# Performance work log

Measured on AMD Instinct MI355X. Metric: run time of the kernel, lower is better.

## Reference

```python
import jax, jax.numpy as jnp
import numpy as np

H, W = 512, 512
NUM_CLASSES = 21
THETA_ALPHA, THETA_BETA, THETA_GAMMA = 80.0, 13.0, 3.0
BILATERAL_COMPAT, SPATIAL_COMPAT = 10.0, 3.0
COMPATIBILITY = -1.0
NUM_ITERATIONS = 5


def _find_rows(rows, queries):
    """Index of each query row in `rows` (lexicographically sorted unique), -1 if absent."""
    M = rows.shape[0]
    u, inv = np.unique(np.concatenate([rows, queries], axis=0), axis=0, return_inverse=True)
    table = np.full(u.shape[0], -1, np.int64)
    table[inv[:M]] = np.arange(M)
    return table[inv[M:]].astype(np.int32)


def _perm_init(feats):
    """Permutohedral lattice init (Adams et al.).
    Returns os [N,d+1] (1-based lattice indices, 0 = pad row), ws [N,d+1] barycentric
    weights, nbrs [d+1,M,2] blur neighbor indices (1-based, 0 = missing)."""
    N, d = feats.shape
    inv_std = np.sqrt(2.0 / 3.0) * (d + 1)
    scale = inv_std / np.sqrt((np.arange(1, d + 1) * np.arange(2, d + 2)).astype(np.float64))
    cf = feats.astype(np.float64) * scale[None]
    # Elevate onto the hyperplane sum(x)=0 in d+1 dims
    E = np.zeros((N, d + 1), np.float64)
    sm = np.zeros(N, np.float64)
    for i in range(d, 0, -1):
        E[:, i] = sm - i * cf[:, i - 1]
        sm = sm + cf[:, i - 1]
    E[:, 0] = sm
    down = 1.0 / (d + 1)
    v = E * down
    up_p = np.ceil(v) * (d + 1)
    dn_p = np.floor(v) * (d + 1)
    rem0 = np.where(up_p - E < E - dn_p, up_p, dn_p)  # nearest remainder-0 point
    sum_ = np.round(rem0.sum(1) * down).astype(np.int64)
    diff = E - rem0
    order = np.argsort(-diff, axis=1, kind='stable')
    rank = np.empty((N, d + 1), np.int64)
    np.put_along_axis(rank, order, np.broadcast_to(np.arange(d + 1, dtype=np.int64), (N, d + 1)).copy(), axis=1)
    rank = rank + sum_[:, None]
    ls = rank < 0
    rank = rank + ls * (d + 1); rem0 = rem0 + ls * (d + 1)
    gt = rank > d
    rank = rank - gt * (d + 1); rem0 = rem0 - gt * (d + 1)
    # Barycentric weights
    bary = np.zeros((N, d + 2), np.float64)
    vv = (E - rem0) * down
    rows_idx = np.arange(N)[:, None]
    np.add.at(bary, (rows_idx, d - rank), vv)
    np.add.at(bary, (rows_idx, d + 1 - rank), -vv)
    bary[:, 0] += 1.0 + bary[:, d + 1]
    ws = bary[:, :d + 1].astype(np.float32)
    # Keys of the d+1 enclosing simplex vertices (first d coords only)
    rem0i = np.round(rem0[:, :d]).astype(np.int32)
    ranks = rank[:, :d]
    keys = np.empty((N, d + 1, d), np.int32)
    for k in range(d + 1):
        keys[:, k, :] = rem0i + np.where(ranks < d + 1 - k, k, k - (d + 1)).astype(np.int32)
    uniq, inv = np.unique(keys.reshape(-1, d), axis=0, return_inverse=True)
    M = uniq.shape[0]
    os_ = (inv.reshape(N, d + 1) + 1).astype(np.int32)
    # Blur neighbors along each lattice direction j
    nbrs = np.zeros((d + 1, M, 2), np.int32)
    for j in range(d + 1):
        n1 = uniq - 1; n2 = uniq + 1
        if j < d:
            n1 = n1.copy(); n2 = n2.copy()
            n1[:, j] += d + 1; n2[:, j] -= d + 1
        nbrs[j, :, 0] = _find_rows(uniq, n1) + 1
        nbrs[j, :, 1] = _find_rows(uniq, n2) + 1
    return os_, ws, nbrs


def setup_inputs() -> dict:
    key = jax.random.key(0)
    k1, k2 = jax.random.split(key)
    unary = jax.random.normal(k1, (H, W, NUM_CLASSES), jnp.float32)
    image = jax.random.uniform(k2, (H, W, 3), jnp.float32) * 255.0  # 0..255 like RGB
    ys, xs = np.meshgrid(np.arange(H, dtype=np.float32), np.arange(W, dtype=np.float32), indexing='ij')
    img = np.asarray(image)
    bifeats = np.concatenate([(xs / THETA_ALPHA)[..., None], (ys / THETA_ALPHA)[..., None], img / THETA_BETA], axis=-1).reshape(-1, 5).astype(np.float32)
    spfeats = np.concatenate([(xs / THETA_GAMMA)[..., None], (ys / THETA_GAMMA)[..., None]], axis=-1).reshape(-1, 2).astype(np.float32)
    os_bi, ws_bi, nbr_bi = _perm_init(bifeats)
    os_sp, ws_sp, nbr_sp = _perm_init(spfeats)
    return {
        'unary': unary,
        'ws_bi': jnp.asarray(ws_bi), 'ws_sp': jnp.asarray(ws_sp),
        'os_bi': jnp.asarray(os_bi), 'os_sp': jnp.asarray(os_sp),
        'nbr_bi': jnp.asarray(nbr_bi), 'nbr_sp': jnp.asarray(nbr_sp),
    }


def lattice_compute(inp, os_, ws, nbrs):
    """Permutohedral splat -> blur -> slice. inp [N,C]; os_ [N,d+1] 1-based;
    ws [N,d+1]; nbrs [d+1,M,2] 1-based with 0 = missing (maps to zero pad row)."""
    N, C = inp.shape
    d = os_.shape[1] - 1
    M = nbrs.shape[1]
    splat = (ws[..., None] * inp[:, None, :]).reshape(-1, C)  # [N*(d+1), C]
    val = jnp.zeros((M + 1, C), inp.dtype).at[os_.reshape(-1)].add(splat)

    def blur(val, nbr_j):
        mixed = val[1:] + 0.5 * (val[nbr_j[:, 0]] + val[nbr_j[:, 1]])
        return val.at[1:].set(mixed), None

    val, _ = jax.lax.scan(blur, val, nbrs)
    alpha = 1.0 / (1.0 + 2.0 ** (-d))
    return alpha * jnp.einsum('nj,njc->nc', ws, val[os_])


def reference(unary, ws_bi, ws_sp, os_bi, os_sp, nbr_bi, nbr_sp):
    N = H * W
    u = unary.reshape(N, NUM_CLASSES)
    ones = jnp.ones((N, 1), jnp.float32)
    bi_norm = 1.0 / (lattice_compute(ones, os_bi, ws_bi, nbr_bi) ** 0.5 + 1e-20)
    sp_norm = 1.0 / (lattice_compute(ones, os_sp, ws_sp, nbr_sp) ** 0.5 + 1e-20)
    Q = jax.nn.softmax(-u, axis=-1)
    for _ in range(NUM_ITERATIONS):
        bi = lattice_compute(Q * bi_norm, os_bi, ws_bi, nbr_bi) * bi_norm
        sp = lattice_compute(Q * sp_norm, os_sp, ws_sp, nbr_sp) * sp_norm
        pairwise = COMPATIBILITY * (BILATERAL_COMPAT * bi + SPATIAL_COMPAT * sp)
        Q = jax.nn.softmax(-u - pairwise, axis=-1)
    return Q.reshape(H, W, NUM_CLASSES)
```

## Files before the change

kernel.cpp:

```cpp
#include <hip/hip_runtime.h>
#include <hip/hip_fp16.h>

#define NPIX (512 * 512)
#define LOG2N 18
#define NC 21
#define CP 11
#define SCAN_CHUNK 2048
#define SCAN_T 256

static inline int cdiv_l(long a, int b) { return (int)((a + b - 1) / b); }

__global__ void hist2_k(const int* __restrict__ osA, int* __restrict__ cntA, int NA, int KA,
                        const int* __restrict__ osB, int* __restrict__ cntB, int NB, int KB) {
    int t = blockIdx.x * blockDim.x + threadIdx.x;
    if (t < NA) {
        int j = t >> LOG2N, n = t & (NPIX - 1);
        atomicAdd(&cntA[osA[(size_t)n * KA + j]], 1);
    } else {
        t -= NA;
        if (t < NB) {
            int j = t >> LOG2N, n = t & (NPIX - 1);
            atomicAdd(&cntB[osB[(size_t)n * KB + j]], 1);
        }
    }
}

__global__ void scan1_k(const int* __restrict__ count, int* __restrict__ bsum, int L) {
    __shared__ int s[SCAN_T];
    int base = blockIdx.x * SCAN_CHUNK;
    int tsum = 0;
    for (int j = threadIdx.x; j < SCAN_CHUNK; j += SCAN_T) {
        int i = base + j;
        tsum += (i < L) ? count[i] : 0;
    }
    s[threadIdx.x] = tsum; __syncthreads();
    for (int o = SCAN_T / 2; o > 0; o >>= 1) {
        if (threadIdx.x < o) s[threadIdx.x] += s[threadIdx.x + o];
        __syncthreads();
    }
    if (threadIdx.x == 0) bsum[blockIdx.x] = s[0];
}

__global__ void scan2_k(int* __restrict__ bsum, int nb, int* __restrict__ off, int L) {
    __shared__ int s[SCAN_T];
    int tid = threadIdx.x;
    int per = (nb + SCAN_T - 1) / SCAN_T;
    int tsum = 0;
    for (int j = 0; j < per; j++) { int i = tid * per + j; if (i < nb) tsum += bsum[i]; }
    s[tid] = tsum; __syncthreads();
    for (int o = 1; o < SCAN_T; o <<= 1) {
        int v = (tid >= o) ? s[tid - o] : 0;
        __syncthreads();
        s[tid] += v;
        __syncthreads();
    }
    int excl = s[tid] - tsum;
    int total = s[SCAN_T - 1];
    int run = excl;
    for (int j = 0; j < per; j++) {
        int i = tid * per + j;
        if (i < nb) { int v = bsum[i]; bsum[i] = run; run += v; }
    }
    if (tid == 0) off[L] = total;
}

__global__ void scan3_k(int* __restrict__ count, const int* __restrict__ bsum,
                        int* __restrict__ off, int L) {
    __shared__ int s[SCAN_T];
    const int PER = SCAN_CHUNK / SCAN_T;
    int tid = threadIdx.x;
    int base = blockIdx.x * SCAN_CHUNK + tid * PER;
    int c[PER];
    int tsum = 0;
#pragma unroll
    for (int j = 0; j < PER; j++) { int i = base + j; c[j] = (i < L) ? count[i] : 0; tsum += c[j]; }
    s[tid] = tsum; __syncthreads();
    for (int o = 1; o < SCAN_T; o <<= 1) {
        int v = (tid >= o) ? s[tid - o] : 0;
        __syncthreads();
        s[tid] += v;
        __syncthreads();
    }
    int run = bsum[blockIdx.x] + s[tid] - tsum;
#pragma unroll
    for (int j = 0; j < PER; j++) {
        int i = base + j;
        if (i < L) { off[i] = run; count[i] = 0; }
        run += c[j];
    }
}

__global__ void scatter2_k(const int* __restrict__ osA, const float* __restrict__ wsA,
                           const int* __restrict__ offA, int* __restrict__ curA,
                           int2* __restrict__ pA, int NA, int KA,
                           const int* __restrict__ osB, const float* __restrict__ wsB,
                           const int* __restrict__ offB, int* __restrict__ curB,
                           int2* __restrict__ pB, int NB, int KB) {
    int t = blockIdx.x * blockDim.x + threadIdx.x;
    if (t < NA) {
        int j = t >> LOG2N, n = t & (NPIX - 1);
        size_t e = (size_t)n * KA + j;
        int m = osA[e];
        int p = offA[m] + atomicAdd(&curA[m], 1);
        pA[p] = make_int2(n, __float_as_int(wsA[e]));
    } else {
        t -= NA;
        if (t < NB) {
            int j = t >> LOG2N, n = t & (NPIX - 1);
            size_t e = (size_t)n * KB + j;
            int m = osB[e];
            int p = offB[m] + atomicAdd(&curB[m], 1);
            pB[p] = make_int2(n, __float_as_int(wsB[e]));
        }
    }
}

__global__ void wn2_k(int2* __restrict__ pA, const float* __restrict__ nrmA, int NA,
                      int2* __restrict__ pB, const float* __restrict__ nrmB, int NB) {
    int t = blockIdx.x * blockDim.x + threadIdx.x;
    if (t < NA) {
        int2 e = pA[t];
        e.y = __float_as_int(__int_as_float(e.y) * nrmA[e.x]);
        pA[t] = e;
    } else {
        t -= NA;
        if (t < NB) {
            int2 e = pB[t];
            e.y = __float_as_int(__int_as_float(e.y) * nrmB[e.x]);
            pB[t] = e;
        }
    }
}

__global__ void splat_gather1_k(const int2* __restrict__ pE, const int* __restrict__ off,
                                float* __restrict__ val, int M) {
    int m = blockIdx.x * blockDim.x + threadIdx.x;
    if (m > M) return;
    float s = 0.f;
    if (m > 0) {
        int e0 = off[m], e1 = off[m + 1];
        for (int e = e0; e < e1; e++) s += __int_as_float(pE[e].y);
    }
    val[m] = s;
}

__global__ void blur1_k(const float* __restrict__ vin, float* __restrict__ vout,
                        const int* __restrict__ nbr, int M) {
    int t = blockIdx.x * blockDim.x + threadIdx.x;
    if (t > M) return;
    if (t == 0) { vout[0] = 0.f; return; }
    int2 nn = ((const int2*)nbr)[t - 1];
    vout[t] = vin[t] + 0.5f * (vin[nn.x] + vin[nn.y]);
}

__global__ void slice_norm_k(const float* __restrict__ ws, const int* __restrict__ os,
                             const float* __restrict__ val, float* __restrict__ nrm,
                             int N, int K, float alpha) {
    int n = blockIdx.x * blockDim.x + threadIdx.x;
    if (n >= N) return;
    float s = 0.f;
    for (int j = 0; j < K; j++) s += ws[(size_t)n * K + j] * val[os[(size_t)n * K + j]];
    nrm[n] = 1.f / (sqrtf(alpha * s) + 1e-20f);
}

__global__ void splatH_k(const __half2* __restrict__ Qh, const int2* __restrict__ pE,
                         const int* __restrict__ off, __half2* __restrict__ val, int M) {
    int m = blockIdx.x * blockDim.x + threadIdx.x;
    if (m > M) return;
    float acc[2 * CP];
#pragma unroll
    for (int i = 0; i < 2 * CP; i++) acc[i] = 0.f;
    if (m > 0) {
        int e0 = off[m], e1 = off[m + 1];
        for (int e = e0; e < e1; e++) {
            int2 ent = pE[e];
            float w = __int_as_float(ent.y);
            const __half2* qp = Qh + (size_t)ent.x * CP;
#pragma unroll
            for (int i = 0; i < CP; i++) {
                float2 q = __half22float2(qp[i]);
                acc[2 * i]     += w * q.x;
                acc[2 * i + 1] += w * q.y;
            }
        }
    }
    __half2* vp = val + (size_t)m * CP;
#pragma unroll
    for (int i = 0; i < CP; i++)
        vp[i] = __floats2half2_rn(acc[2 * i], acc[2 * i + 1]);
}

__global__ void blurH_k(const __half2* __restrict__ vin, __half2* __restrict__ vout,
                        const int* __restrict__ nbr, int M) {
    int t = blockIdx.x * blockDim.x + threadIdx.x;
    int total = (M + 1) * CP;
    if (t >= total) return;
    int m = t / CP;
    int cp = t - m * CP;
    if (m == 0) { vout[t] = __floats2half2_rn(0.f, 0.f); return; }
    int2 nn = ((const int2*)nbr)[m - 1];
    float2 a = __half22float2(vin[t]);
    float2 b = __half22float2(vin[(size_t)nn.x * CP + cp]);
    float2 c = __half22float2(vin[(size_t)nn.y * CP + cp]);
    vout[t] = __floats2half2_rn(a.x + 0.5f * (b.x + c.x), a.y + 0.5f * (b.y + c.y));
}

__global__ void blurH2_k(const __half2* __restrict__ vin, __half2* __restrict__ vout,
                         const int* __restrict__ nbrA, const int* __restrict__ nbrB, int M) {
    int m = blockIdx.x * blockDim.x + threadIdx.x;
    if (m > M) return;
    __half2* op = vout + (size_t)m * CP;
    if (m == 0) {
        __half2 z = __floats2half2_rn(0.f, 0.f);
#pragma unroll
        for (int i = 0; i < CP; i++) op[i] = z;
        return;
    }
    float acc[2 * CP];
#pragma unroll
    for (int i = 0; i < 2 * CP; i++) acc[i] = 0.f;
    int2 nbB = ((const int2*)nbrB)[m - 1];

    {
        int2 na = ((const int2*)nbrA)[m - 1];
        const __half2* p0 = vin + (size_t)m * CP;
        const __half2* p1 = vin + (size_t)na.x * CP;
        const __half2* p2 = vin + (size_t)na.y * CP;
#pragma unroll
        for (int i = 0; i < CP; i++) {
            float2 a = __half22float2(p0[i]);
            float2 b = __half22float2(p1[i]);
            float2 c = __half22float2(p2[i]);
            acc[2 * i]     += a.x + 0.5f * (b.x + c.x);
            acc[2 * i + 1] += a.y + 0.5f * (b.y + c.y);
        }
    }
    if (nbB.x > 0) {
        int2 na = ((const int2*)nbrA)[nbB.x - 1];
        const __half2* p0 = vin + (size_t)nbB.x * CP;
        const __half2* p1 = vin + (size_t)na.x * CP;
        const __half2* p2 = vin + (size_t)na.y * CP;
#pragma unroll
        for (int i = 0; i < CP; i++) {
            float2 a = __half22float2(p0[i]);
            float2 b = __half22float2(p1[i]);
            float2 c = __half22float2(p2[i]);
            acc[2 * i]     += 0.5f * (a.x + 0.5f * (b.x + c.x));
            acc[2 * i + 1] += 0.5f * (a.y + 0.5f * (b.y + c.y));
        }
    }
    if (nbB.y > 0) {
        int2 na = ((const int2*)nbrA)[nbB.y - 1];
        const __half2* p0 = vin + (size_t)nbB.y * CP;
        const __half2* p1 = vin + (size_t)na.x * CP;
        const __half2* p2 = vin + (size_t)na.y * CP;
#pragma unroll
        for (int i = 0; i < CP; i++) {
            float2 a = __half22float2(p0[i]);
            float2 b = __half22float2(p1[i]);
            float2 c = __half22float2(p2[i]);
            acc[2 * i]     += 0.5f * (a.x + 0.5f * (b.x + c.x));
            acc[2 * i + 1] += 0.5f * (a.y + 0.5f * (b.y + c.y));
        }
    }
#pragma unroll
    for (int i = 0; i < CP; i++)
        op[i] = __floats2half2_rn(acc[2 * i], acc[2 * i + 1]);
}

__global__ void softmax_init_k(const float* __restrict__ u, __half2* __restrict__ Qh,
                               __half2* __restrict__ uh, int N) {
    int n = blockIdx.x * blockDim.x + threadIdx.x;
    if (n >= N) return;
    const float* up = u + (size_t)n * NC;
    float uv[2 * CP], v[2 * CP];
    float mx = -1e30f;
#pragma unroll
    for (int c = 0; c < NC; c++) { uv[c] = up[c]; v[c] = -uv[c]; mx = fmaxf(mx, v[c]); }
    float s = 0.f;
#pragma unroll
    for (int c = 0; c < NC; c++) { v[c] = __expf(v[c] - mx); s += v[c]; }
    float inv = 1.f / s;
#pragma unroll
    for (int c = 0; c < NC; c++) v[c] *= inv;
    v[NC] = 0.f; uv[NC] = 0.f;
    __half2* hp = Qh + (size_t)n * CP;
    __half2* uhp = uh + (size_t)n * CP;
#pragma unroll
    for (int i = 0; i < CP; i++) {
        hp[i]  = __floats2half2_rn(v[2 * i], v[2 * i + 1]);
        uhp[i] = __floats2half2_rn(uv[2 * i], uv[2 * i + 1]);
    }
}

__global__ void slice_update_k(const __half2* __restrict__ uh,
                               const int* __restrict__ os_bi, const float* __restrict__ ws_bi,
                               const __half2* __restrict__ vbi, const float* __restrict__ nrm_bi,
                               const int* __restrict__ os_sp, const float* __restrict__ ws_sp,
                               const __half2* __restrict__ vsp, const float* __restrict__ nrm_sp,
                               float* __restrict__ Q, __half2* __restrict__ Qh,
                               int N, float abi, float asp, int final_it) {
    int n = blockIdx.x * blockDim.x + threadIdx.x;
    if (n >= N) return;
    float acc[2 * CP];
#pragma unroll
    for (int i = 0; i < 2 * CP; i++) acc[i] = 0.f;
    for (int j = 0; j < 6; j++) {
        float w = ws_bi[(size_t)n * 6 + j];
        const __half2* vp = vbi + (size_t)os_bi[(size_t)n * 6 + j] * CP;
#pragma unroll
        for (int i = 0; i < CP; i++) {
            float2 f = __half22float2(vp[i]);
            acc[2 * i]     += w * f.x;
            acc[2 * i + 1] += w * f.y;
        }
    }
    float sb = 10.f * abi * nrm_bi[n];
#pragma unroll
    for (int i = 0; i < 2 * CP; i++) acc[i] *= sb;
    float ss = 3.f * asp * nrm_sp[n];
    for (int j = 0; j < 3; j++) {
        float w = ss * ws_sp[(size_t)n * 3 + j];
        const __half2* vp = vsp + (size_t)os_sp[(size_t)n * 3 + j] * CP;
#pragma unroll
        for (int i = 0; i < CP; i++) {
            float2 f = __half22float2(vp[i]);
            acc[2 * i]     += w * f.x;
            acc[2 * i + 1] += w * f.y;
        }
    }
    const __half2* uhp = uh + (size_t)n * CP;
#pragma unroll
    for (int i = 0; i < CP; i++) {
        float2 uu = __half22float2(uhp[i]);
        acc[2 * i]     -= uu.x;
        acc[2 * i + 1] -= uu.y;
    }
    float mx = -1e30f;
#pragma unroll
    for (int c = 0; c < NC; c++) mx = fmaxf(mx, acc[c]);
    float s = 0.f;
#pragma unroll
    for (int c = 0; c < NC; c++) { acc[c] = __expf(acc[c] - mx); s += acc[c]; }
    float inv = 1.f / s;
#pragma unroll
    for (int c = 0; c < NC; c++) acc[c] *= inv;
    acc[NC] = 0.f;
    if (final_it) {
        float* qp = Q + (size_t)n * NC;
#pragma unroll
        for (int c = 0; c < NC; c++) qp[c] = acc[c];
    } else {
        __half2* hp = Qh + (size_t)n * CP;
#pragma unroll
        for (int i = 0; i < CP; i++) hp[i] = __floats2half2_rn(acc[2 * i], acc[2 * i + 1]);
    }
}

extern "C" void kernel_launch(void* const* d_in, const int* in_sizes, int n_in,
                              void* d_out, int out_size, void* d_ws, size_t ws_size,
                              hipStream_t stream) {
    const float* unary  = (const float*)d_in[0];
    const float* ws_bi  = (const float*)d_in[1];
    const float* ws_sp  = (const float*)d_in[2];
    const int*   os_bi  = (const int*)d_in[3];
    const int*   os_sp  = (const int*)d_in[4];
    const int*   nbr_bi = (const int*)d_in[5];
    const int*   nbr_sp = (const int*)d_in[6];
    float* Q = (float*)d_out;

    const int N = NPIX, Kbi = 6, Ksp = 3;
    const int Mbi = in_sizes[5] / (Kbi * 2);
    const int Msp = in_sizes[6] / (Ksp * 2);
    const int NKbi = N * Kbi, NKsp = N * Ksp;
    const float alpha_bi = 32.f / 33.f;
    const float alpha_sp = 0.8f;

    char* basec = (char*)d_ws;
    size_t off4 = 0;
    auto allocf = [&](size_t nf) { float* p = (float*)basec + off4; off4 += (nf + 3) & ~(size_t)3; return p; };
    auto alloci = [&](size_t ni) { int* p = (int*)basec + off4; off4 += (ni + 3) & ~(size_t)3; return p; };
    auto alloch2 = [&](size_t nh2) { __half2* p = (__half2*)((float*)basec + off4); off4 += (nh2 + 3) & ~(size_t)3; return p; };
    auto alloci2 = [&](size_t ni2) { int2* p = (int2*)((float*)basec + off4); off4 += 2 * ni2; return p; };

    float*   nrm_bi = allocf(N);
    float*   nrm_sp = allocf(N);
    __half2* Qh     = alloch2((size_t)N * CP);
    __half2* uh     = alloch2((size_t)N * CP);
    int2*    pE_bi  = alloci2(NKbi);
    int*     off_bi = alloci(Mbi + 2);
    int2*    pE_sp  = alloci2(NKsp);
    int*     off_sp = alloci(Msp + 2);
    int*     cur_bi = alloci((size_t)(Mbi + 1) + (Msp + 1));
    int*     cur_sp = cur_bi + (Mbi + 1);
    int*     bsum   = alloci(4096);
    __half2* vbiA   = alloch2((size_t)(Mbi + 1) * CP);
    __half2* vbiB   = alloch2((size_t)(Mbi + 1) * CP);
    __half2* vspA   = alloch2((size_t)(Msp + 1) * CP);
    __half2* vspB   = alloch2((size_t)(Msp + 1) * CP);
    float* nv_biA = (float*)vbiA;
    float* nv_biB = (float*)vbiB;
    float* nv_spA = (float*)vspA;
    float* nv_spB = (float*)vspB;

    const int B = 256;
    const int nb_bi = cdiv_l(Mbi + 1, SCAN_CHUNK);
    const int nb_sp = cdiv_l(Msp + 1, SCAN_CHUNK);
    const size_t cur_span = ((size_t)(Mbi + 1) + (Msp + 1)) * sizeof(int);

    hipMemsetAsync(cur_bi, 0, cur_span, stream);
    hist2_k<<<cdiv_l((long)NKbi + NKsp, B), B, 0, stream>>>(
        os_bi, cur_bi, NKbi, Kbi, os_sp, cur_sp, NKsp, Ksp);
    scan1_k<<<nb_bi, SCAN_T, 0, stream>>>(cur_bi, bsum, Mbi + 1);
    scan2_k<<<1, SCAN_T, 0, stream>>>(bsum, nb_bi, off_bi, Mbi + 1);
    scan3_k<<<nb_bi, SCAN_T, 0, stream>>>(cur_bi, bsum, off_bi, Mbi + 1);
    scan1_k<<<nb_sp, SCAN_T, 0, stream>>>(cur_sp, bsum, Msp + 1);
    scan2_k<<<1, SCAN_T, 0, stream>>>(bsum, nb_sp, off_sp, Msp + 1);
    scan3_k<<<nb_sp, SCAN_T, 0, stream>>>(cur_sp, bsum, off_sp, Msp + 1);
    scatter2_k<<<cdiv_l((long)NKbi + NKsp, B), B, 0, stream>>>(
        os_bi, ws_bi, off_bi, cur_bi, pE_bi, NKbi, Kbi,
        os_sp, ws_sp, off_sp, cur_sp, pE_sp, NKsp, Ksp);

    splat_gather1_k<<<cdiv_l(Mbi + 1, B), B, 0, stream>>>(pE_bi, off_bi, nv_biA, Mbi);
    {
        float* s = nv_biA; float* d = nv_biB;
        for (int j = 0; j < Kbi; j++) {
            blur1_k<<<cdiv_l(Mbi + 1, B), B, 0, stream>>>(s, d, nbr_bi + (size_t)j * Mbi * 2, Mbi);
            float* t = s; s = d; d = t;
        }
        slice_norm_k<<<cdiv_l(N, B), B, 0, stream>>>(ws_bi, os_bi, s, nrm_bi, N, Kbi, alpha_bi);
    }

    splat_gather1_k<<<cdiv_l(Msp + 1, B), B, 0, stream>>>(pE_sp, off_sp, nv_spA, Msp);
    {
        float* s = nv_spA; float* d = nv_spB;
        for (int j = 0; j < Ksp; j++) {
            blur1_k<<<cdiv_l(Msp + 1, B), B, 0, stream>>>(s, d, nbr_sp + (size_t)j * Msp * 2, Msp);
            float* t = s; s = d; d = t;
        }
        slice_norm_k<<<cdiv_l(N, B), B, 0, stream>>>(ws_sp, os_sp, s, nrm_sp, N, Ksp, alpha_sp);
    }

    wn2_k<<<cdiv_l((long)NKbi + NKsp, B), B, 0, stream>>>(pE_bi, nrm_bi, NKbi, pE_sp, nrm_sp, NKsp);

    softmax_init_k<<<cdiv_l(N, B), B, 0, stream>>>(unary, Qh, uh, N);

    for (int it = 0; it < 5; it++) {
        splatH_k<<<cdiv_l(Mbi + 1, B), B, 0, stream>>>(Qh, pE_bi, off_bi, vbiA, Mbi);
        blurH2_k<<<cdiv_l(Mbi + 1, B), B, 0, stream>>>(
            vbiA, vbiB, nbr_bi + (size_t)0 * Mbi * 2, nbr_bi + (size_t)1 * Mbi * 2, Mbi);
        blurH2_k<<<cdiv_l(Mbi + 1, B), B, 0, stream>>>(
            vbiB, vbiA, nbr_bi + (size_t)2 * Mbi * 2, nbr_bi + (size_t)3 * Mbi * 2, Mbi);
        blurH2_k<<<cdiv_l(Mbi + 1, B), B, 0, stream>>>(
            vbiA, vbiB, nbr_bi + (size_t)4 * Mbi * 2, nbr_bi + (size_t)5 * Mbi * 2, Mbi);
        splatH_k<<<cdiv_l(Msp + 1, B), B, 0, stream>>>(Qh, pE_sp, off_sp, vspA, Msp);
        blurH2_k<<<cdiv_l(Msp + 1, B), B, 0, stream>>>(
            vspA, vspB, nbr_sp + (size_t)0 * Msp * 2, nbr_sp + (size_t)1 * Msp * 2, Msp);
        blurH_k<<<cdiv_l((long)(Msp + 1) * CP, B), B, 0, stream>>>(
            vspB, vspA, nbr_sp + (size_t)2 * Msp * 2, Msp);
        slice_update_k<<<cdiv_l(N, B), B, 0, stream>>>(
            uh, os_bi, ws_bi, vbiB, nrm_bi, os_sp, ws_sp, vspA, nrm_sp,
            Q, Qh, N, alpha_bi, alpha_sp, it == 4 ? 1 : 0);
    }
}
```

Baseline: 1.258 ms.

## Merge bilateral and spatial lattice kernels and compact splat entries

Bilateral and spatial lattice passes (scan, splat, blur, normalization, softmax init) now run together in shared launches instead of separate ones, which cuts the kernel count per iteration and fills the GPU better for the smaller spatial lattice. Splat entries shrink from int2 (pixel, prenormalized weight) to a packed int (pixel<<3|vertex). The weight and norm are re-read and multiplied inside the splat, which removes the wn2 pass at the cost of extra gathers from ws and nrm in every iteration.

```diff
diff --git a/kernel.cpp b/kernel.cpp
--- a/kernel.cpp
+++ b/kernel.cpp
@@ -25,24 +25,33 @@
     }
 }
 
-__global__ void scan1_k(const int* __restrict__ count, int* __restrict__ bsum, int L) {
+__global__ void scan1d_k(const int* __restrict__ cntA, int* __restrict__ bsumA, int LA, int nbA,
+                         const int* __restrict__ cntB, int* __restrict__ bsumB, int LB) {
     __shared__ int s[SCAN_T];
-    int base = blockIdx.x * SCAN_CHUNK;
+    int blk = blockIdx.x;
+    const int* cnt; int* bsum; int L; int b;
+    if (blk < nbA) { cnt = cntA; bsum = bsumA; L = LA; b = blk; }
+    else           { cnt = cntB; bsum = bsumB; L = LB; b = blk - nbA; }
+    int base = b * SCAN_CHUNK;
     int tsum = 0;
     for (int j = threadIdx.x; j < SCAN_CHUNK; j += SCAN_T) {
         int i = base + j;
-        tsum += (i < L) ? count[i] : 0;
+        tsum += (i < L) ? cnt[i] : 0;
     }
     s[threadIdx.x] = tsum; __syncthreads();
     for (int o = SCAN_T / 2; o > 0; o >>= 1) {
         if (threadIdx.x < o) s[threadIdx.x] += s[threadIdx.x + o];
         __syncthreads();
     }
-    if (threadIdx.x == 0) bsum[blockIdx.x] = s[0];
-}
-
-__global__ void scan2_k(int* __restrict__ bsum, int nb, int* __restrict__ off, int L) {
+    if (threadIdx.x == 0) bsum[b] = s[0];
+}
+
+__global__ void scan2d_k(int* __restrict__ bsumA, int nbA, int* __restrict__ offA, int LA,
+                         int* __restrict__ bsumB, int nbB, int* __restrict__ offB, int LB) {
     __shared__ int s[SCAN_T];
+    int* bsum; int nb; int* off; int L;
+    if (blockIdx.x == 0) { bsum = bsumA; nb = nbA; off = offA; L = LA; }
+    else                 { bsum = bsumB; nb = nbB; off = offB; L = LB; }
     int tid = threadIdx.x;
     int per = (nb + SCAN_T - 1) / SCAN_T;
     int tsum = 0;
@@ -64,16 +73,22 @@
     if (tid == 0) off[L] = total;
 }
 
-__global__ void scan3_k(int* __restrict__ count, const int* __restrict__ bsum,
-                        int* __restrict__ off, int L) {
+__global__ void scan3d_k(int* __restrict__ cntA, const int* __restrict__ bsumA, int* __restrict__ offA,
+                         int LA, int nbA,
+                         int* __restrict__ cntB, const int* __restrict__ bsumB, int* __restrict__ offB,
+                         int LB) {
     __shared__ int s[SCAN_T];
     const int PER = SCAN_CHUNK / SCAN_T;
+    int blk = blockIdx.x;
+    int* cnt; const int* bsum; int* off; int L; int b;
+    if (blk < nbA) { cnt = cntA; bsum = bsumA; off = offA; L = LA; b = blk; }
+    else           { cnt = cntB; bsum = bsumB; off = offB; L = LB; b = blk - nbA; }
     int tid = threadIdx.x;
-    int base = blockIdx.x * SCAN_CHUNK + tid * PER;
+    int base = b * SCAN_CHUNK + tid * PER;
     int c[PER];
     int tsum = 0;
 #pragma unroll
-    for (int j = 0; j < PER; j++) { int i = base + j; c[j] = (i < L) ? count[i] : 0; tsum += c[j]; }
+    for (int j = 0; j < PER; j++) { int i = base + j; c[j] = (i < L) ? cnt[i] : 0; tsum += c[j]; }
     s[tid] = tsum; __syncthreads();
     for (int o = 1; o < SCAN_T; o <<= 1) {
         int v = (tid >= o) ? s[tid - o] : 0;
@@ -81,101 +96,133 @@
         s[tid] += v;
         __syncthreads();
     }
-    int run = bsum[blockIdx.x] + s[tid] - tsum;
+    int run = bsum[b] + s[tid] - tsum;
 #pragma unroll
     for (int j = 0; j < PER; j++) {
         int i = base + j;
-        if (i < L) { off[i] = run; count[i] = 0; }
+        if (i < L) { off[i] = run; cnt[i] = 0; }
         run += c[j];
     }
 }
 
-__global__ void scatter2_k(const int* __restrict__ osA, const float* __restrict__ wsA,
-                           const int* __restrict__ offA, int* __restrict__ curA,
-                           int2* __restrict__ pA, int NA, int KA,
-                           const int* __restrict__ osB, const float* __restrict__ wsB,
-                           const int* __restrict__ offB, int* __restrict__ curB,
-                           int2* __restrict__ pB, int NB, int KB) {
+__global__ void scatter2_k(const int* __restrict__ osA, const int* __restrict__ offA,
+                           int* __restrict__ curA, int* __restrict__ pA, int NA, int KA,
+                           const int* __restrict__ osB, const int* __restrict__ offB,
+                           int* __restrict__ curB, int* __restrict__ pB, int NB, int KB) {
     int t = blockIdx.x * blockDim.x + threadIdx.x;
     if (t < NA) {
         int j = t >> LOG2N, n = t & (NPIX - 1);
-        size_t e = (size_t)n * KA + j;
-        int m = osA[e];
+        int m = osA[(size_t)n * KA + j];
         int p = offA[m] + atomicAdd(&curA[m], 1);
-        pA[p] = make_int2(n, __float_as_int(wsA[e]));
+        pA[p] = (n << 3) | j;
     } else {
         t -= NA;
         if (t < NB) {
             int j = t >> LOG2N, n = t & (NPIX - 1);
-            size_t e = (size_t)n * KB + j;
-            int m = osB[e];
+            int m = osB[(size_t)n * KB + j];
             int p = offB[m] + atomicAdd(&curB[m], 1);
-            pB[p] = make_int2(n, __float_as_int(wsB[e]));
-        }
-    }
-}
-
-__global__ void wn2_k(int2* __restrict__ pA, const float* __restrict__ nrmA, int NA,
-                      int2* __restrict__ pB, const float* __restrict__ nrmB, int NB) {
-    int t = blockIdx.x * blockDim.x + threadIdx.x;
-    if (t < NA) {
-        int2 e = pA[t];
-        e.y = __float_as_int(__int_as_float(e.y) * nrmA[e.x]);
-        pA[t] = e;
-    } else {
-        t -= NA;
-        if (t < NB) {
-            int2 e = pB[t];
-            e.y = __float_as_int(__int_as_float(e.y) * nrmB[e.x]);
-            pB[t] = e;
-        }
-    }
-}
-
-__global__ void splat_gather1_k(const int2* __restrict__ pE, const int* __restrict__ off,
-                                float* __restrict__ val, int M) {
-    int m = blockIdx.x * blockDim.x + threadIdx.x;
-    if (m > M) return;
+            pB[p] = (n << 3) | j;
+        }
+    }
+}
+
+__global__ void splat1d_k(const int* __restrict__ pE_bi, const int* __restrict__ off_bi,
+                          const float* __restrict__ ws_bi, float* __restrict__ val_bi, int Mbi,
+                          const int* __restrict__ pE_sp, const int* __restrict__ off_sp,
+                          const float* __restrict__ ws_sp, float* __restrict__ val_sp, int Msp) {
+    int t = blockIdx.x * blockDim.x + threadIdx.x;
+    const int* pE; const int* off; const float* ws; float* val; int m, K;
+    if (t <= Mbi) { pE = pE_bi; off = off_bi; ws = ws_bi; val = val_bi; m = t; K = 6; }
+    else {
+        m = t - (Mbi + 1);
+        if (m > Msp) return;
+        pE = pE_sp; off = off_sp; ws = ws_sp; val = val_sp; K = 3;
+    }
     float s = 0.f;
     if (m > 0) {
         int e0 = off[m], e1 = off[m + 1];
-        for (int e = e0; e < e1; e++) s += __int_as_float(pE[e].y);
+        for (int e = e0; e < e1; e++) {
+            int un = pE[e];
+            s += ws[(size_t)(un >> 3) * K + (un & 7)];
+        }
     }
     val[m] = s;
 }
 
-__global__ void blur1_k(const float* __restrict__ vin, float* __restrict__ vout,
-                        const int* __restrict__ nbr, int M) {
-    int t = blockIdx.x * blockDim.x + threadIdx.x;
-    if (t > M) return;
-    if (t == 0) { vout[0] = 0.f; return; }
-    int2 nn = ((const int2*)nbr)[t - 1];
-    vout[t] = vin[t] + 0.5f * (vin[nn.x] + vin[nn.y]);
-}
-
-__global__ void slice_norm_k(const float* __restrict__ ws, const int* __restrict__ os,
-                             const float* __restrict__ val, float* __restrict__ nrm,
-                             int N, int K, float alpha) {
-    int n = blockIdx.x * blockDim.x + threadIdx.x;
-    if (n >= N) return;
-    float s = 0.f;
-    for (int j = 0; j < K; j++) s += ws[(size_t)n * K + j] * val[os[(size_t)n * K + j]];
-    nrm[n] = 1.f / (sqrtf(alpha * s) + 1e-20f);
-}
-
-__global__ void splatH_k(const __half2* __restrict__ Qh, const int2* __restrict__ pE,
-                         const int* __restrict__ off, __half2* __restrict__ val, int M) {
-    int m = blockIdx.x * blockDim.x + threadIdx.x;
-    if (m > M) return;
+__global__ void blur1d_k(const float* __restrict__ biIn, float* __restrict__ biOut,
+                         const int* __restrict__ nbr_bi, int Mbi,
+                         const float* __restrict__ spIn, float* __restrict__ spOut,
+                         const int* __restrict__ nbr_sp, int Msp) {
+    int t = blockIdx.x * blockDim.x + threadIdx.x;
+    if (t <= Mbi) {
+        if (t == 0) { biOut[0] = 0.f; return; }
+        int2 nn = ((const int2*)nbr_bi)[t - 1];
+        biOut[t] = biIn[t] + 0.5f * (biIn[nn.x] + biIn[nn.y]);
+    } else if (spIn) {
+        int m = t - (Mbi + 1);
+        if (m > Msp) return;
+        if (m == 0) { spOut[0] = 0.f; return; }
+        int2 nn = ((const int2*)nbr_sp)[m - 1];
+        spOut[m] = spIn[m] + 0.5f * (spIn[nn.x] + spIn[nn.y]);
+    }
+}
+
+__global__ void prep_k(const float* __restrict__ unary,
+                       const int* __restrict__ os_bi, const float* __restrict__ ws_bi,
+                       const float* __restrict__ nv_bi, float* __restrict__ nrm_bi, float abi,
+                       const int* __restrict__ os_sp, const float* __restrict__ ws_sp,
+                       const float* __restrict__ nv_sp, float* __restrict__ nrm_sp, float asp,
+                       __half2* __restrict__ Qh, __half2* __restrict__ uh, int N) {
+    int t = blockIdx.x * blockDim.x + threadIdx.x;
+    if (t < N) {
+        float s = 0.f;
+        for (int j = 0; j < 6; j++)
+            s += ws_bi[(size_t)t * 6 + j] * nv_bi[os_bi[(size_t)t * 6 + j]];
+        nrm_bi[t] = 1.f / (sqrtf(abi * s) + 1e-20f);
+    } else if (t < 2 * N) {
+        int n = t - N;
+        float s = 0.f;
+        for (int j = 0; j < 3; j++)
+            s += ws_sp[(size_t)n * 3 + j] * nv_sp[os_sp[(size_t)n * 3 + j]];
+        nrm_sp[n] = 1.f / (sqrtf(asp * s) + 1e-20f);
+    } else if (t < 3 * N) {
+        int n = t - 2 * N;
+        const float* up = unary + (size_t)n * NC;
+        float uv[2 * CP], v[2 * CP];
+        float mx = -1e30f;
+#pragma unroll
+        for (int c = 0; c < NC; c++) { uv[c] = up[c]; v[c] = -uv[c]; mx = fmaxf(mx, v[c]); }
+        float s = 0.f;
+#pragma unroll
+        for (int c = 0; c < NC; c++) { v[c] = __expf(v[c] - mx); s += v[c]; }
+        float inv = 1.f / s;
+#pragma unroll
+        for (int c = 0; c < NC; c++) v[c] *= inv;
+        v[NC] = 0.f; uv[NC] = 0.f;
+        __half2* hp = Qh + (size_t)n * CP;
+        __half2* uhp = uh + (size_t)n * CP;
+#pragma unroll
+        for (int i = 0; i < CP; i++) {
+            hp[i]  = __floats2half2_rn(v[2 * i], v[2 * i + 1]);
+            uhp[i] = __floats2half2_rn(uv[2 * i], uv[2 * i + 1]);
+        }
+    }
+}
+
+__device__ __forceinline__ void splat_row(const __half2* __restrict__ Qh,
+                                          const int* __restrict__ pE, const int* __restrict__ off,
+                                          const float* __restrict__ ws, const float* __restrict__ nrm,
+                                          __half2* __restrict__ val, int m, int K) {
     float acc[2 * CP];
 #pragma unroll
     for (int i = 0; i < 2 * CP; i++) acc[i] = 0.f;
     if (m > 0) {
         int e0 = off[m], e1 = off[m + 1];
         for (int e = e0; e < e1; e++) {
-            int2 ent = pE[e];
-            float w = __int_as_float(ent.y);
-            const __half2* qp = Qh + (size_t)ent.x * CP;
+            int un = pE[e];
+            int n = un >> 3, j = un & 7;
+            float w = ws[(size_t)n * K + j] * nrm[n];
+            const __half2* qp = Qh + (size_t)n * CP;
 #pragma unroll
             for (int i = 0; i < CP; i++) {
                 float2 q = __half22float2(qp[i]);
@@ -190,26 +237,26 @@
         vp[i] = __floats2half2_rn(acc[2 * i], acc[2 * i + 1]);
 }
 
-__global__ void blurH_k(const __half2* __restrict__ vin, __half2* __restrict__ vout,
-                        const int* __restrict__ nbr, int M) {
-    int t = blockIdx.x * blockDim.x + threadIdx.x;
-    int total = (M + 1) * CP;
-    if (t >= total) return;
-    int m = t / CP;
-    int cp = t - m * CP;
-    if (m == 0) { vout[t] = __floats2half2_rn(0.f, 0.f); return; }
-    int2 nn = ((const int2*)nbr)[m - 1];
-    float2 a = __half22float2(vin[t]);
-    float2 b = __half22float2(vin[(size_t)nn.x * CP + cp]);
-    float2 c = __half22float2(vin[(size_t)nn.y * CP + cp]);
-    vout[t] = __floats2half2_rn(a.x + 0.5f * (b.x + c.x), a.y + 0.5f * (b.y + c.y));
-}
-
-__global__ void blurH2_k(const __half2* __restrict__ vin, __half2* __restrict__ vout,
-                         const int* __restrict__ nbrA, const int* __restrict__ nbrB, int M) {
-    int m = blockIdx.x * blockDim.x + threadIdx.x;
-    if (m > M) return;
-    __half2* op = vout + (size_t)m * CP;
+__global__ void splatH2_k(const __half2* __restrict__ Qh,
+                          const int* __restrict__ pE_bi, const int* __restrict__ off_bi,
+                          const float* __restrict__ ws_bi, const float* __restrict__ nrm_bi,
+                          __half2* __restrict__ val_bi, int Mbi,
+                          const int* __restrict__ pE_sp, const int* __restrict__ off_sp,
+                          const float* __restrict__ ws_sp, const float* __restrict__ nrm_sp,
+                          __half2* __restrict__ val_sp, int Msp) {
+    int t = blockIdx.x * blockDim.x + threadIdx.x;
+    if (t <= Mbi) {
+        splat_row(Qh, pE_bi, off_bi, ws_bi, nrm_bi, val_bi, t, 6);
+    } else {
+        int m = t - (Mbi + 1);
+        if (m > Msp) return;
+        splat_row(Qh, pE_sp, off_sp, ws_sp, nrm_sp, val_sp, m, 3);
+    }
+}
+
+__device__ __forceinline__ void blur2_row(const __half2* __restrict__ vin, __half2* __restrict__ op,
+                                          const int* __restrict__ nbrA, const int* __restrict__ nbrB,
+                                          int m) {
     if (m == 0) {
         __half2 z = __floats2half2_rn(0.f, 0.f);
 #pragma unroll
@@ -220,7 +267,6 @@
 #pragma unroll
     for (int i = 0; i < 2 * CP; i++) acc[i] = 0.f;
     int2 nbB = ((const int2*)nbrB)[m - 1];
-
     {
         int2 na = ((const int2*)nbrA)[m - 1];
         const __half2* p0 = vin + (size_t)m * CP;
@@ -268,29 +314,60 @@
         op[i] = __floats2half2_rn(acc[2 * i], acc[2 * i + 1]);
 }
 
-__global__ void softmax_init_k(const float* __restrict__ u, __half2* __restrict__ Qh,
-                               __half2* __restrict__ uh, int N) {
-    int n = blockIdx.x * blockDim.x + threadIdx.x;
-    if (n >= N) return;
-    const float* up = u + (size_t)n * NC;
-    float uv[2 * CP], v[2 * CP];
-    float mx = -1e30f;
-#pragma unroll
-    for (int c = 0; c < NC; c++) { uv[c] = up[c]; v[c] = -uv[c]; mx = fmaxf(mx, v[c]); }
-    float s = 0.f;
-#pragma unroll
-    for (int c = 0; c < NC; c++) { v[c] = __expf(v[c] - mx); s += v[c]; }
-    float inv = 1.f / s;
-#pragma unroll
-    for (int c = 0; c < NC; c++) v[c] *= inv;
-    v[NC] = 0.f; uv[NC] = 0.f;
-    __half2* hp = Qh + (size_t)n * CP;
-    __half2* uhp = uh + (size_t)n * CP;
+__device__ __forceinline__ void blur1_row(const __half2* __restrict__ vin, __half2* __restrict__ op,
+                                          const int* __restrict__ nbr, int m) {
+    if (m == 0) {
+        __half2 z = __floats2half2_rn(0.f, 0.f);
+#pragma unroll
+        for (int i = 0; i < CP; i++) op[i] = z;
+        return;
+    }
+    int2 nn = ((const int2*)nbr)[m - 1];
+    const __half2* p0 = vin + (size_t)m * CP;
+    const __half2* p1 = vin + (size_t)nn.x * CP;
+    const __half2* p2 = vin + (size_t)nn.y * CP;
 #pragma unroll
     for (int i = 0; i < CP; i++) {
-        hp[i]  = __floats2half2_rn(v[2 * i], v[2 * i + 1]);
-        uhp[i] = __floats2half2_rn(uv[2 * i], uv[2 * i + 1]);
-    }
+        float2 a = __half22float2(p0[i]);
+        float2 b = __half22float2(p1[i]);
+        float2 c = __half22float2(p2[i]);
+        op[i] = __floats2half2_rn(a.x + 0.5f * (b.x + c.x), a.y + 0.5f * (b.y + c.y));
+    }
+}
+
+__global__ void blurP1_k(const __half2* __restrict__ biIn, __half2* __restrict__ biOut,
+                         const int* __restrict__ nA_bi, const int* __restrict__ nB_bi, int Mbi,
+                         const __half2* __restrict__ spIn, __half2* __restrict__ spOut,
+                         const int* __restrict__ nA_sp, const int* __restrict__ nB_sp, int Msp) {
+    int t = blockIdx.x * blockDim.x + threadIdx.x;
+    if (t <= Mbi) {
+        blur2_row(biIn, biOut + (size_t)t * CP, nA_bi, nB_bi, t);
+    } else {
+        int m = t - (Mbi + 1);
+        if (m > Msp) return;
+        blur2_row(spIn, spOut + (size_t)m * CP, nA_sp, nB_sp, m);
+    }
+}
+
+__global__ void blurP2_k(const __half2* __restrict__ biIn, __half2* __restrict__ biOut,
+                         const int* __restrict__ nA_bi, const int* __restrict__ nB_bi, int Mbi,
+                         const __half2* __restrict__ spIn, __half2* __restrict__ spOut,
+                         const int* __restrict__ nA_sp, int Msp) {
+    int t = blockIdx.x * blockDim.x + threadIdx.x;
+    if (t <= Mbi) {
+        blur2_row(biIn, biOut + (size_t)t * CP, nA_bi, nB_bi, t);
+    } else {
+        int m = t - (Mbi + 1);
+        if (m > Msp) return;
+        blur1_row(spIn, spOut + (size_t)m * CP, nA_sp, m);
+    }
+}
+
+__global__ void blurP3_k(const __half2* __restrict__ biIn, __half2* __restrict__ biOut,
+                         const int* __restrict__ nA_bi, const int* __restrict__ nB_bi, int Mbi) {
+    int t = blockIdx.x * blockDim.x + threadIdx.x;
+    if (t > Mbi) return;
+    blur2_row(biIn, biOut + (size_t)t * CP, nA_bi, nB_bi, t);
 }
 
 __global__ void slice_update_k(const __half2* __restrict__ uh,
@@ -381,19 +458,19 @@
     auto allocf = [&](size_t nf) { float* p = (float*)basec + off4; off4 += (nf + 3) & ~(size_t)3; return p; };
     auto alloci = [&](size_t ni) { int* p = (int*)basec + off4; off4 += (ni + 3) & ~(size_t)3; return p; };
     auto alloch2 = [&](size_t nh2) { __half2* p = (__half2*)((float*)basec + off4); off4 += (nh2 + 3) & ~(size_t)3; return p; };
-    auto alloci2 = [&](size_t ni2) { int2* p = (int2*)((float*)basec + off4); off4 += 2 * ni2; return p; };
 
     float*   nrm_bi = allocf(N);
     float*   nrm_sp = allocf(N);
     __half2* Qh     = alloch2((size_t)N * CP);
     __half2* uh     = alloch2((size_t)N * CP);
-    int2*    pE_bi  = alloci2(NKbi);
+    int*     pE_bi  = alloci(NKbi);
     int*     off_bi = alloci(Mbi + 2);
-    int2*    pE_sp  = alloci2(NKsp);
+    int*     pE_sp  = alloci(NKsp);
     int*     off_sp = alloci(Msp + 2);
     int*     cur_bi = alloci((size_t)(Mbi + 1) + (Msp + 1));
     int*     cur_sp = cur_bi + (Mbi + 1);
-    int*     bsum   = alloci(4096);
+    int*     bsumA  = alloci(4096);
+    int*     bsumB  = alloci(4096);
     __half2* vbiA   = alloch2((size_t)(Mbi + 1) * CP);
     __half2* vbiB   = alloch2((size_t)(Mbi + 1) * CP);
     __half2* vspA   = alloch2((size_t)(Msp + 1) * CP);
@@ -407,57 +484,56 @@
     const int nb_bi = cdiv_l(Mbi + 1, SCAN_CHUNK);
     const int nb_sp = cdiv_l(Msp + 1, SCAN_CHUNK);
     const size_t cur_span = ((size_t)(Mbi + 1) + (Msp + 1)) * sizeof(int);
+    const int rows2 = (Mbi + 1) + (Msp + 1);
 
     hipMemsetAsync(cur_bi, 0, cur_span, stream);
     hist2_k<<<cdiv_l((long)NKbi + NKsp, B), B, 0, stream>>>(
         os_bi, cur_bi, NKbi, Kbi, os_sp, cur_sp, NKsp, Ksp);
-    scan1_k<<<nb_bi, SCAN_T, 0, stream>>>(cur_bi, bsum, Mbi + 1);
-    scan2_k<<<1, SCAN_T, 0, stream>>>(bsum, nb_bi, off_bi, Mbi + 1);
-    scan3_k<<<nb_bi, SCAN_T, 0, stream>>>(cur_bi, bsum, off_bi, Mbi + 1);
-    scan1_k<<<nb_sp, SCAN_T, 0, stream>>>(cur_sp, bsum, Msp + 1);
-    scan2_k<<<1, SCAN_T, 0, stream>>>(bsum, nb_sp, off_sp, Msp + 1);
-    scan3_k<<<nb_sp, SCAN_T, 0, stream>>>(cur_sp, bsum, off_sp, Msp + 1);
+    scan1d_k<<<nb_bi + nb_sp, SCAN_T, 0, stream>>>(cur_bi, bsumA, Mbi + 1, nb_bi,
+                                                   cur_sp, bsumB, Msp + 1);
+    scan2d_k<<<2, SCAN_T, 0, stream>>>(bsumA, nb_bi, off_bi, Mbi + 1,
+                                       bsumB, nb_sp, off_sp, Msp + 1);
+    scan3d_k<<<nb_bi + nb_sp, SCAN_T, 0, stream>>>(cur_bi, bsumA, off_bi, Mbi + 1, nb_bi,
+                                                   cur_sp, bsumB, off_sp, Msp + 1);
     scatter2_k<<<cdiv_l((long)NKbi + NKsp, B), B, 0, stream>>>(
-        os_bi, ws_bi, off_bi, cur_bi, pE_bi, NKbi, Kbi,
-        os_sp, ws_sp, off_sp, cur_sp, pE_sp, NKsp, Ksp);
-
-    splat_gather1_k<<<cdiv_l(Mbi + 1, B), B, 0, stream>>>(pE_bi, off_bi, nv_biA, Mbi);
+        os_bi, off_bi, cur_bi, pE_bi, NKbi, Kbi,
+        os_sp, off_sp, cur_sp, pE_sp, NKsp, Ksp);
+
+    splat1d_k<<<cdiv_l(rows2, B), B, 0, stream>>>(pE_bi, off_bi, ws_bi, nv_biA, Mbi,
+                                                  pE_sp, off_sp, ws_sp, nv_spA, Msp);
     {
-        float* s = nv_biA; float* d = nv_biB;
-        for (int j = 0; j < Kbi; j++) {
-            blur1_k<<<cdiv_l(Mbi + 1, B), B, 0, stream>>>(s, d, nbr_bi + (size_t)j * Mbi * 2, Mbi);
-            float* t = s; s = d; d = t;
-        }
-        slice_norm_k<<<cdiv_l(N, B), B, 0, stream>>>(ws_bi, os_bi, s, nrm_bi, N, Kbi, alpha_bi);
-    }
-
-    splat_gather1_k<<<cdiv_l(Msp + 1, B), B, 0, stream>>>(pE_sp, off_sp, nv_spA, Msp);
-    {
-        float* s = nv_spA; float* d = nv_spB;
-        for (int j = 0; j < Ksp; j++) {
-            blur1_k<<<cdiv_l(Msp + 1, B), B, 0, stream>>>(s, d, nbr_sp + (size_t)j * Msp * 2, Msp);
-            float* t = s; s = d; d = t;
-        }
-        slice_norm_k<<<cdiv_l(N, B), B, 0, stream>>>(ws_sp, os_sp, s, nrm_sp, N, Ksp, alpha_sp);
-    }
-
-    wn2_k<<<cdiv_l((long)NKbi + NKsp, B), B, 0, stream>>>(pE_bi, nrm_bi, NKbi, pE_sp, nrm_sp, NKsp);
-
-    softmax_init_k<<<cdiv_l(N, B), B, 0, stream>>>(unary, Qh, uh, N);
+        float* sb = nv_biA; float* db = nv_biB;
+        float* sp = nv_spA; float* dp = nv_spB;
+        for (int j = 0; j < 3; j++) {
+            blur1d_k<<<cdiv_l(rows2, B), B, 0, stream>>>(
+                sb, db, nbr_bi + (size_t)j * Mbi * 2, Mbi,
+                sp, dp, nbr_sp + (size_t)j * Msp * 2, Msp);
+            float* t = sb; sb = db; db = t;
+            t = sp; sp = dp; dp = t;
+        }
+        for (int j = 3; j < 6; j++) {
+            blur1d_k<<<cdiv_l(Mbi + 1, B), B, 0, stream>>>(
+                sb, db, nbr_bi + (size_t)j * Mbi * 2, Mbi,
+                nullptr, nullptr, nullptr, 0);
+            float* t = sb; sb = db; db = t;
+        }
+        prep_k<<<cdiv_l(3L * N, B), B, 0, stream>>>(
+            unary, os_bi, ws_bi, sb, nrm_bi, alpha_bi,
+            os_sp, ws_sp, sp, nrm_sp, alpha_sp, Qh, uh, N);
+    }
 
     for (int it = 0; it < 5; it++) {
-        splatH_k<<<cdiv_l(Mbi + 1, B), B, 0, stream>>>(Qh, pE_bi, off_bi, vbiA, Mbi);
-        blurH2_k<<<cdiv_l(Mbi + 1, B), B, 0, stream>>>(
-            vbiA, vbiB, nbr_bi + (size_t)0 * Mbi * 2, nbr_bi + (size_t)1 * Mbi * 2, Mbi);
-        blurH2_k<<<cdiv_l(Mbi + 1, B), B, 0, stream>>>(
-            vbiB, vbiA, nbr_bi + (size_t)2 * Mbi * 2, nbr_bi + (size_t)3 * Mbi * 2, Mbi);
-        blurH2_k<<<cdiv_l(Mbi + 1, B), B, 0, stream>>>(
+        splatH2_k<<<cdiv_l(rows2, B), B, 0, stream>>>(
+            Qh, pE_bi, off_bi, ws_bi, nrm_bi, vbiA, Mbi,
+            pE_sp, off_sp, ws_sp, nrm_sp, vspA, Msp);
+        blurP1_k<<<cdiv_l(rows2, B), B, 0, stream>>>(
+            vbiA, vbiB, nbr_bi + (size_t)0 * Mbi * 2, nbr_bi + (size_t)1 * Mbi * 2, Mbi,
+            vspA, vspB, nbr_sp + (size_t)0 * Msp * 2, nbr_sp + (size_t)1 * Msp * 2, Msp);
+        blurP2_k<<<cdiv_l(rows2, B), B, 0, stream>>>(
+            vbiB, vbiA, nbr_bi + (size_t)2 * Mbi * 2, nbr_bi + (size_t)3 * Mbi * 2, Mbi,
+            vspB, vspA, nbr_sp + (size_t)2 * Msp * 2, Msp);
+        blurP3_k<<<cdiv_l(Mbi + 1, B), B, 0, stream>>>(
             vbiA, vbiB, nbr_bi + (size_t)4 * Mbi * 2, nbr_bi + (size_t)5 * Mbi * 2, Mbi);
-        splatH_k<<<cdiv_l(Msp + 1, B), B, 0, stream>>>(Qh, pE_sp, off_sp, vspA, Msp);
-        blurH2_k<<<cdiv_l(Msp + 1, B), B, 0, stream>>>(
-            vspA, vspB, nbr_sp + (size_t)0 * Msp * 2, nbr_sp + (size_t)1 * Msp * 2, Msp);
-        blurH_k<<<cdiv_l((long)(Msp + 1) * CP, B), B, 0, stream>>>(
-            vspB, vspA, nbr_sp + (size_t)2 * Msp * 2, Msp);
         slice_update_k<<<cdiv_l(N, B), B, 0, stream>>>(
             uh, os_bi, ws_bi, vbiB, nrm_bi, os_sp, ws_sp, vspA, nrm_sp,
             Q, Qh, N, alpha_bi, alpha_sp, it == 4 ? 1 : 0);
```

After: 1.389 ms. +10.4%, slower.
